# Kernel tuning notes

Hardware: AMD Instinct MI355X
Metric: run time of the kernel (lower is better)

The kernel has to match this reference:

```python
import jax, jax.numpy as jnp
import numpy as np

NUM_HEADS = 16
HEAD_DIM = 128  # 2048 / 16


def setup_inputs() -> dict:
    key = jax.random.key(0)
    ks = jax.random.split(key, 5)
    B, S, D = 2, 2048, 2048
    scale = 1.0 / np.sqrt(D)
    return {
        "x": jax.random.normal(ks[0], (B, S, D), dtype=jnp.float32),
        "Wq": jax.random.normal(ks[1], (D, D), dtype=jnp.float32) * scale,
        "Wk": jax.random.normal(ks[2], (D, D), dtype=jnp.float32) * scale,
        "Wv": jax.random.normal(ks[3], (D, D), dtype=jnp.float32) * scale,
        "Wo": jax.random.normal(ks[4], (D, D), dtype=jnp.float32) * scale,
    }


def reference(x, Wq, Wk, Wv, Wo):
    B, S, D = x.shape
    H, Hd = NUM_HEADS, HEAD_DIM
    # nn.Linear(bias=False): y = x @ W.T
    q = (x @ Wq.T).reshape(B, S, H, Hd).transpose(0, 2, 1, 3)  # [B,H,S,Hd]
    k = (x @ Wk.T).reshape(B, S, H, Hd).transpose(0, 2, 1, 3)
    v = (x @ Wv.T).reshape(B, S, H, Hd).transpose(0, 2, 1, 3)
    scores = jnp.einsum("bhqd,bhkd->bhqk", q, k) / jnp.sqrt(jnp.float32(Hd))
    attn = jax.nn.softmax(scores, axis=-1)  # dropout p=0 (eval) -> identity
    out = jnp.einsum("bhqk,bhkd->bhqd", attn, v)  # [B,H,S,Hd]
    out = out.transpose(0, 2, 1, 3).reshape(B, S, D)
    out = out @ Wo.T
    return out
```

## Files before the change

### kernel.cpp

```cpp
#include <hip/hip_runtime.h>
#include <math.h>
#include <stdint.h>


#define DDIM 2048
#define SEQ  2048
#define NH   16
#define HD   128

typedef __attribute__((ext_vector_type(4))) float f32x4;
typedef __attribute__((ext_vector_type(16))) float f32x16;
typedef __attribute__((ext_vector_type(8))) __bf16 bf16x8;
typedef __attribute__((ext_vector_type(4))) unsigned int u32x4;
typedef __attribute__((ext_vector_type(2))) unsigned int u32x2;

#define MFMA_B16(a, b, c) __builtin_amdgcn_mfma_f32_16x16x32_bf16((a), (b), (c), 0, 0, 0)
#define MFMA32(a, b, c) __builtin_amdgcn_mfma_f32_32x32x16_bf16((a), (b), (c), 0, 0, 0)

__device__ __forceinline__ void async16(const void* g, void* l) {
  __builtin_amdgcn_global_load_lds(
      (const __attribute__((address_space(1))) unsigned int*)g,
      (__attribute__((address_space(3))) unsigned int*)l, 16, 0, 0);
}

__device__ __forceinline__ unsigned short f2bf(float f) {
  unsigned u = __builtin_bit_cast(unsigned, f);
  u += 0x7fffu + ((u >> 16) & 1u);
  return (unsigned short)(u >> 16);
}

__device__ __forceinline__ bf16x8 ldfrag(const unsigned short* p) {
  return __builtin_bit_cast(bf16x8, *(const u32x4*)p);
}

__device__ __forceinline__ void cvt_body(const float* __restrict__ s,
                                         unsigned short* __restrict__ d, int i) {
  const f32x4* sp = (const f32x4*)s;
  f32x4 a = sp[2 * i], b = sp[2 * i + 1];
  u32x4 o;
  o.x = ((unsigned)f2bf(a.y) << 16) | f2bf(a.x);
  o.y = ((unsigned)f2bf(a.w) << 16) | f2bf(a.z);
  o.z = ((unsigned)f2bf(b.y) << 16) | f2bf(b.x);
  o.w = ((unsigned)f2bf(b.w) << 16) | f2bf(b.z);
  ((u32x4*)d)[i] = o;
}

__global__ __launch_bounds__(256) void cvt_bf16_kernel(const float* __restrict__ s,
                                                       unsigned short* __restrict__ d) {
  cvt_body(s, d, blockIdx.x * 256 + threadIdx.x);
}

__global__ __launch_bounds__(256) void cvt_all_kernel(const float* __restrict__ x,
                                                      const float* __restrict__ wq,
                                                      const float* __restrict__ wk,
                                                      const float* __restrict__ wv,
                                                      const float* __restrict__ wo,
                                                      unsigned short* __restrict__ xb,
                                                      unsigned short* __restrict__ wqkv,
                                                      unsigned short* __restrict__ wob) {
  const int b = blockIdx.x;
  if (b < 4096) {
    cvt_body(x, xb, b * 256 + threadIdx.x);
  } else if (b < 10240) {
    const int wi = (b - 4096) >> 11, lb = (b - 4096) & 2047;
    const float* s = (wi == 0) ? wq : (wi == 1) ? wk : wv;
    cvt_body(s, wqkv + (size_t)wi * 4194304u, lb * 256 + threadIdx.x);
  } else {
    cvt_body(wo, wob, (b - 10240) * 256 + threadIdx.x);
  }
}

__global__ __launch_bounds__(256) void gemm_qkv(const unsigned short* __restrict__ A,
                                                const unsigned short* __restrict__ B,
                                                unsigned short* __restrict__ Oqk,
                                                unsigned short* __restrict__ Ovt,
                                                float alpha_q) {
  __shared__ unsigned short As[128 * 64];
  __shared__ unsigned short Bs[128 * 64];
  const int tid = threadIdx.x;
  const int lane = tid & 63, w = tid >> 6;
  const int l32 = lane & 31, half = lane >> 5;
  const int wm = (w >> 1) * 64, wn = (w & 1) * 64;
  const int bm = blockIdx.y * 128, bn = blockIdx.x * 128;

  f32x16 acc[2][2];
#pragma unroll
  for (int i = 0; i < 2; ++i)
#pragma unroll
    for (int j = 0; j < 2; ++j)
#pragma unroll
      for (int e = 0; e < 16; ++e) acc[i][j][e] = 0.f;

  const unsigned short* pa[4];
  const unsigned short* pbb[4];
  {
#pragma unroll
    for (int j = 0; j < 4; ++j) {
      const int row = j * 32 + (tid >> 3);
      const int cg = (tid & 7) ^ (row & 7) ^ ((row >> 3) & 7);
      pa[j] = A + (size_t)(bm + row) * DDIM + cg * 8;
      pbb[j] = B + (size_t)(bn + row) * DDIM + cg * 8;
    }
  }

  const int fr = (l32 & 7) ^ (l32 >> 3);

  for (int kt = 0; kt < 32; ++kt) {
    __syncthreads();
#pragma unroll
    for (int j = 0; j < 4; ++j) {
      async16(pa[j], &As[(j * 256 + tid) * 8]);
      pa[j] += 64;
      async16(pbb[j], &Bs[(j * 256 + tid) * 8]);
      pbb[j] += 64;
    }
    __syncthreads();
#pragma unroll
    for (int ks = 0; ks < 4; ++ks) {
      const int ph = ks * 2 + half;
      const int sl0 = (ph ^ fr) * 8;
      const int sl1 = (ph ^ fr ^ 4) * 8;
      bf16x8 af0 = ldfrag(&As[(wm + l32) * 64 + sl0]);
      bf16x8 af1 = ldfrag(&As[(wm + 32 + l32) * 64 + sl1]);
      bf16x8 bf0 = ldfrag(&Bs[(wn + l32) * 64 + sl0]);
      bf16x8 bf1 = ldfrag(&Bs[(wn + 32 + l32) * 64 + sl1]);
      acc[0][0] = MFMA32(af0, bf0, acc[0][0]);
      acc[0][1] = MFMA32(af0, bf1, acc[0][1]);
      acc[1][0] = MFMA32(af1, bf0, acc[1][0]);
      acc[1][1] = MFMA32(af1, bf1, acc[1][1]);
    }
  }

  const int seg = bn >> 11;
  const int bnl = bn & 2047;
  const float alpha = (seg == 0) ? alpha_q : 1.0f;
#pragma unroll
  for (int i = 0; i < 2; ++i) {
#pragma unroll
    for (int j = 0; j < 2; ++j) {
#pragma unroll
      for (int rg = 0; rg < 4; ++rg) {
        const int m0 = bm + wm + i * 32 + rg * 8 + half * 4;
        const float v0 = acc[i][j][rg * 4 + 0] * alpha;
        const float v1 = acc[i][j][rg * 4 + 1] * alpha;
        const float v2 = acc[i][j][rg * 4 + 2] * alpha;
        const float v3 = acc[i][j][rg * 4 + 3] * alpha;
        const int n = bnl + wn + j * 32 + l32;
        if (seg < 2) {
          unsigned short* O = Oqk + (size_t)seg * (4096u * 2048u);
          O[(size_t)(m0 + 0) * DDIM + n] = f2bf(v0);
          O[(size_t)(m0 + 1) * DDIM + n] = f2bf(v1);
          O[(size_t)(m0 + 2) * DDIM + n] = f2bf(v2);
          O[(size_t)(m0 + 3) * DDIM + n] = f2bf(v3);
        } else {
          const int bb = m0 >> 11, s0 = m0 & 2047;
          const int hh = n >> 7, dd = n & 127;
          u32x2 st;
          st.x = ((unsigned)f2bf(v1) << 16) | f2bf(v0);
          st.y = ((unsigned)f2bf(v3) << 16) | f2bf(v2);
          *(u32x2*)&Ovt[((size_t)((bb * NH + hh) * HD + dd)) * SEQ + s0] = st;
        }
      }
    }
  }
}

__global__ __launch_bounds__(256) void gemm_o64(const unsigned short* __restrict__ A,
                                                const unsigned short* __restrict__ B,
                                                float* __restrict__ Cf) {
  __shared__ unsigned short As[128 * 64];
  __shared__ unsigned short Bs[64 * 64];
  const int tid = threadIdx.x;
  const int lane = tid & 63, w = tid >> 6;
  const int l32 = lane & 31, half = lane >> 5;
  const int wm = (w >> 1) * 64, wn = (w & 1) * 32;
  const int bm = blockIdx.y * 128, bn = blockIdx.x * 64;

  f32x16 acc[2];
#pragma unroll
  for (int i = 0; i < 2; ++i)
#pragma unroll
    for (int e = 0; e < 16; ++e) acc[i][e] = 0.f;

  const unsigned short* pa[4];
  const unsigned short* pbb[2];
  {
#pragma unroll
    for (int j = 0; j < 4; ++j) {
      const int row = j * 32 + (tid >> 3);
      const int cg = (tid & 7) ^ (row & 7) ^ ((row >> 3) & 7);
      pa[j] = A + (size_t)(bm + row) * DDIM + cg * 8;
      if (j < 2) pbb[j] = B + (size_t)(bn + row) * DDIM + cg * 8;
    }
  }

  const int fr = (l32 & 7) ^ (l32 >> 3);
  const int fb = fr ^ ((wn >> 3) & 4);

  for (int kt = 0; kt < 32; ++kt) {
    __syncthreads();
#pragma unroll
    for (int j = 0; j < 4; ++j) {
      async16(pa[j], &As[(j * 256 + tid) * 8]);
      pa[j] += 64;
      if (j < 2) {
        async16(pbb[j], &Bs[(j * 256 + tid) * 8]);
        pbb[j] += 64;
      }
    }
    __syncthreads();
#pragma unroll
    for (int ks = 0; ks < 4; ++ks) {
      const int ph = ks * 2 + half;
      bf16x8 af0 = ldfrag(&As[(wm + l32) * 64 + (ph ^ fr) * 8]);
      bf16x8 af1 = ldfrag(&As[(wm + 32 + l32) * 64 + (ph ^ fr ^ 4) * 8]);
      bf16x8 bf0 = ldfrag(&Bs[(wn + l32) * 64 + (ph ^ fb) * 8]);
      acc[0] = MFMA32(af0, bf0, acc[0]);
      acc[1] = MFMA32(af1, bf0, acc[1]);
    }
  }

#pragma unroll
  for (int i = 0; i < 2; ++i) {
#pragma unroll
    for (int rg = 0; rg < 4; ++rg) {
      const int m0 = bm + wm + i * 32 + rg * 8 + half * 4;
      const int n = bn + wn + l32;
      Cf[(size_t)(m0 + 0) * DDIM + n] = acc[i][rg * 4 + 0];
      Cf[(size_t)(m0 + 1) * DDIM + n] = acc[i][rg * 4 + 1];
      Cf[(size_t)(m0 + 2) * DDIM + n] = acc[i][rg * 4 + 2];
      Cf[(size_t)(m0 + 3) * DDIM + n] = acc[i][rg * 4 + 3];
    }
  }
}

__global__ __launch_bounds__(512) void attn_kernel(const unsigned short* __restrict__ qb,
                                                   const unsigned short* __restrict__ kb,
                                                   const unsigned short* __restrict__ vtb,
                                                   unsigned short* __restrict__ ab) {
  __shared__ unsigned short Ks[64 * 128];
  __shared__ unsigned short Vts[128 * 64];
  __shared__ unsigned short Pw[8 * 16 * 40];
  const int tid = threadIdx.x;
  const int w = tid >> 6, lane = tid & 63;
  const int quad = lane >> 4, l16 = lane & 15;
  const int qt = blockIdx.x, bh = blockIdx.y;
  const int b = bh >> 4, h = bh & 15;
  const int qrow = qt * 128 + w * 16 + l16;

  const unsigned short* qp = qb + ((size_t)(b * SEQ + qrow)) * DDIM + h * HD;
  bf16x8 qf[4];
#pragma unroll
  for (int ks = 0; ks < 4; ++ks) qf[ks] = ldfrag(qp + ks * 32 + quad * 8);

  f32x4 ot[8];
#pragma unroll
  for (int i = 0; i < 8; i++) ot[i] = f32x4{0.f, 0.f, 0.f, 0.f};
  float sumacc = 0.f;

  const unsigned short* kp[2];
  const unsigned short* vp[2];
  {
    const size_t kbase = ((size_t)(b * SEQ)) * DDIM + h * HD;
    const size_t vbase = ((size_t)((b * NH + h) * HD)) * SEQ;
#pragma unroll
    for (int j = 0; j < 2; ++j) {
      const int key = j * 32 + (tid >> 4), cgk = (tid & 15) ^ (key & 15);
      kp[j] = kb + kbase + (size_t)key * DDIM + cgk * 8;
      const int dd = j * 64 + (tid >> 3), cgv = (tid & 7) ^ (dd & 7);
      vp[j] = vtb + vbase + (size_t)dd * SEQ + cgv * 8;
    }
  }
  unsigned short* pw = &Pw[w * 640];

  for (int kt = 0; kt < SEQ / 64; ++kt) {
    __syncthreads();
#pragma unroll
    for (int j = 0; j < 2; ++j) {
      async16(kp[j], &Ks[(j * 512 + tid) * 8]);
      kp[j] += (size_t)64 * DDIM;
      async16(vp[j], &Vts[(j * 512 + tid) * 8]);
      vp[j] += 64;
    }
    __syncthreads();
    f32x4 s[4];
#pragma unroll
    for (int t = 0; t < 4; ++t) s[t] = f32x4{0.f, 0.f, 0.f, 0.f};
#pragma unroll
    for (int ks = 0; ks < 4; ++ks) {
      const int sl = ((ks * 4 + quad) ^ l16) * 8;
#pragma unroll
      for (int t = 0; t < 4; ++t) {
        bf16x8 a = ldfrag(&Ks[(t * 16 + l16) * 128 + sl]);
        s[t] = MFMA_B16(a, qf[ks], s[t]);
      }
    }
    f32x4 p[4];
#pragma unroll
    for (int t = 0; t < 4; ++t) {
      p[t].x = __builtin_amdgcn_exp2f(s[t].x);
      p[t].y = __builtin_amdgcn_exp2f(s[t].y);
      p[t].z = __builtin_amdgcn_exp2f(s[t].z);
      p[t].w = __builtin_amdgcn_exp2f(s[t].w);
      sumacc += (p[t].x + p[t].y) + (p[t].z + p[t].w);
    }
    bf16x8 pb0, pb1;
    {
      u32x2 w0, w1;
      w0.x = ((unsigned)f2bf(p[0].y) << 16) | f2bf(p[0].x);
      w0.y = ((unsigned)f2bf(p[0].w) << 16) | f2bf(p[0].z);
      w1.x = ((unsigned)f2bf(p[1].y) << 16) | f2bf(p[1].x);
      w1.y = ((unsigned)f2bf(p[1].w) << 16) | f2bf(p[1].z);
      *(u32x2*)&pw[l16 * 40 + quad * 4] = w0;
      *(u32x2*)&pw[l16 * 40 + 16 + quad * 4] = w1;
      asm volatile("s_waitcnt lgkmcnt(0)" ::: "memory");
      pb0 = ldfrag(&pw[l16 * 40 + quad * 8]);
      w0.x = ((unsigned)f2bf(p[2].y) << 16) | f2bf(p[2].x);
      w0.y = ((unsigned)f2bf(p[2].w) << 16) | f2bf(p[2].z);
      w1.x = ((unsigned)f2bf(p[3].y) << 16) | f2bf(p[3].x);
      w1.y = ((unsigned)f2bf(p[3].w) << 16) | f2bf(p[3].z);
      *(u32x2*)&pw[l16 * 40 + quad * 4] = w0;
      *(u32x2*)&pw[l16 * 40 + 16 + quad * 4] = w1;
      asm volatile("s_waitcnt lgkmcnt(0)" ::: "memory");
      pb1 = ldfrag(&pw[l16 * 40 + quad * 8]);
    }
#pragma unroll
    for (int mt = 0; mt < 8; ++mt) {
      bf16x8 vf0 = ldfrag(&Vts[(mt * 16 + l16) * 64 + (quad ^ (l16 & 7)) * 8]);
      ot[mt] = MFMA_B16(vf0, pb0, ot[mt]);
      bf16x8 vf1 = ldfrag(&Vts[(mt * 16 + l16) * 64 + ((4 + quad) ^ (l16 & 7)) * 8]);
      ot[mt] = MFMA_B16(vf1, pb1, ot[mt]);
    }
  }
  float total = sumacc;
  total += __shfl_xor(total, 16);
  total += __shfl_xor(total, 32);
  const float inv = 1.0f / total;
  unsigned short* op = ab + ((size_t)(b * SEQ + qrow)) * DDIM + h * HD;
#pragma unroll
  for (int mt = 0; mt < 8; ++mt) {
    f32x4 v = ot[mt] * inv;
    u32x2 st;
    st.x = ((unsigned)f2bf(v.y) << 16) | f2bf(v.x);
    st.y = ((unsigned)f2bf(v.w) << 16) | f2bf(v.z);
    *(u32x2*)&op[mt * 16 + quad * 4] = st;
  }
}

extern "C" void kernel_launch(void* const* d_in, const int* in_sizes, int n_in,
                              void* d_out, int out_size, void* d_ws, size_t ws_size,
                              hipStream_t stream) {
  (void)in_sizes; (void)n_in; (void)out_size;
  const float* x = (const float*)d_in[0];
  const float* Wq = (const float*)d_in[1];
  const float* Wk = (const float*)d_in[2];
  const float* Wv = (const float*)d_in[3];
  const float* Wo = (const float*)d_in[4];

  char* ws = (char*)d_ws;
  unsigned short* xb = (unsigned short*)(ws);
  unsigned short* wqkv = (unsigned short*)(ws + 16777216);
  unsigned short* qb = (unsigned short*)(ws + 41943040);
  unsigned short* kb = (unsigned short*)(ws + 58720256);
  unsigned short* vtb = (unsigned short*)(ws + 75497472);
  const bool big = ws_size >= 100663296ull;
  unsigned short* wob = big ? (unsigned short*)(ws + 92274688) : wqkv;

  const float alpha_q = 1.44269504088896341f / sqrtf(128.0f);

  if (big) {
    cvt_all_kernel<<<dim3(12288), 256, 0, stream>>>(x, Wq, Wk, Wv, Wo, xb, wqkv, wob);
    gemm_qkv<<<dim3(48, 32), 256, 0, stream>>>(xb, wqkv, qb, vtb, alpha_q);
  } else {
    cvt_all_kernel<<<dim3(10240), 256, 0, stream>>>(x, Wq, Wk, Wv, Wo, xb, wqkv, wob);
    gemm_qkv<<<dim3(48, 32), 256, 0, stream>>>(xb, wqkv, qb, vtb, alpha_q);
    cvt_bf16_kernel<<<dim3(2048), 256, 0, stream>>>(Wo, wob);
  }

  attn_kernel<<<dim3(16, 32), 512, 0, stream>>>(qb, kb, vtb, xb);

  gemm_o64<<<dim3(32, 32), 256, 0, stream>>>(xb, wob, (float*)d_out);
}
```

Baseline: 366.8 us.

## Rewrite QKV GEMM as 256x256 8-wave kernel with ping-pong LDS pipelining

```diff
diff --git a/kernel.cpp b/kernel.cpp
--- a/kernel.cpp
+++ b/kernel.cpp
@@ -70,82 +70,130 @@
   }
 }
 
-__global__ __launch_bounds__(256) void gemm_qkv(const unsigned short* __restrict__ A,
-                                                const unsigned short* __restrict__ B,
-                                                unsigned short* __restrict__ Oqk,
-                                                unsigned short* __restrict__ Ovt,
-                                                float alpha_q) {
-  __shared__ unsigned short As[128 * 64];
-  __shared__ unsigned short Bs[128 * 64];
+#define STGA(BUF, KH, COL)                            \
+  {                                                   \
+    const int c_ = (COL) & 2047;                      \
+    async16(pA[0] + c_, &As[BUF][KH][tid * 8]);       \
+    async16(pA[1] + c_, &As[BUF][KH][4096 + tid * 8]);\
+  }
+#define STGB(BUF, KH, COL)                            \
+  {                                                   \
+    const int c_ = (COL) & 2047;                      \
+    async16(pB[0] + c_, &Bs[BUF][KH][tid * 8]);       \
+    async16(pB[1] + c_, &Bs[BUF][KH][4096 + tid * 8]);\
+  }
+#define VM8 asm volatile("s_waitcnt vmcnt(8)" ::: "memory")
+#define VMNONE (void)0
+
+#define PHASE(BUF, KH, NH, STAGE_STMT, WAIT_STMT)                 \
+  {                                                               \
+    if ((NH) == 0) {                                              \
+      const unsigned short* pl = &As[BUF][KH][0];                 \
+      _Pragma("unroll") for (int mf = 0; mf < 4; ++mf) {          \
+        const int r = awbase + mf * 32;                           \
+        af[mf][0] = ldfrag(pl + r * 32 + c0);                     \
+        af[mf][1] = ldfrag(pl + r * 32 + c1);                     \
+      }                                                           \
+    }                                                             \
+    {                                                             \
+      const unsigned short* pl = &Bs[BUF][KH][0];                 \
+      const int r = bwbase + (NH) * 32;                           \
+      bf0 = ldfrag(pl + r * 32 + c0);                             \
+      bf1 = ldfrag(pl + r * 32 + c1);                             \
+    }                                                             \
+    STAGE_STMT;                                                   \
+    __builtin_amdgcn_s_barrier();                                 \
+    asm volatile("s_waitcnt lgkmcnt(0)" ::: "memory");            \
+    __builtin_amdgcn_sched_barrier(0);                            \
+    __builtin_amdgcn_s_setprio(1);                                \
+    _Pragma("unroll") for (int mf = 0; mf < 4; ++mf) {            \
+      acc[mf][NH] = MFMA32(af[mf][0], bf0, acc[mf][NH]);          \
+      acc[mf][NH] = MFMA32(af[mf][1], bf1, acc[mf][NH]);          \
+    }                                                             \
+    __builtin_amdgcn_s_setprio(0);                                \
+    WAIT_STMT;                                                    \
+    __builtin_amdgcn_s_barrier();                                 \
+  }
+
+__global__ __launch_bounds__(512) void gemm_qkv8(const unsigned short* __restrict__ A,
+                                                 const unsigned short* __restrict__ B,
+                                                 unsigned short* __restrict__ Oqk,
+                                                 unsigned short* __restrict__ Ovt,
+                                                 float alpha_q) {
+  __shared__ unsigned short As[2][2][256 * 32];
+  __shared__ unsigned short Bs[2][2][256 * 32];
   const int tid = threadIdx.x;
   const int lane = tid & 63, w = tid >> 6;
   const int l32 = lane & 31, half = lane >> 5;
-  const int wm = (w >> 1) * 64, wn = (w & 1) * 64;
-  const int bm = blockIdx.y * 128, bn = blockIdx.x * 128;
-
-  f32x16 acc[2][2];
-#pragma unroll
-  for (int i = 0; i < 2; ++i)
-#pragma unroll
-    for (int j = 0; j < 2; ++j)
-#pragma unroll
-      for (int e = 0; e < 16; ++e) acc[i][j][e] = 0.f;
-
-  const unsigned short* pa[4];
-  const unsigned short* pbb[4];
-  {
-#pragma unroll
-    for (int j = 0; j < 4; ++j) {
-      const int row = j * 32 + (tid >> 3);
-      const int cg = (tid & 7) ^ (row & 7) ^ ((row >> 3) & 7);
-      pa[j] = A + (size_t)(bm + row) * DDIM + cg * 8;
-      pbb[j] = B + (size_t)(bn + row) * DDIM + cg * 8;
-    }
-  }
-
-  const int fr = (l32 & 7) ^ (l32 >> 3);
-
-  for (int kt = 0; kt < 32; ++kt) {
-    __syncthreads();
-#pragma unroll
-    for (int j = 0; j < 4; ++j) {
-      async16(pa[j], &As[(j * 256 + tid) * 8]);
-      pa[j] += 64;
-      async16(pbb[j], &Bs[(j * 256 + tid) * 8]);
-      pbb[j] += 64;
-    }
-    __syncthreads();
-#pragma unroll
-    for (int ks = 0; ks < 4; ++ks) {
-      const int ph = ks * 2 + half;
-      const int sl0 = (ph ^ fr) * 8;
-      const int sl1 = (ph ^ fr ^ 4) * 8;
-      bf16x8 af0 = ldfrag(&As[(wm + l32) * 64 + sl0]);
-      bf16x8 af1 = ldfrag(&As[(wm + 32 + l32) * 64 + sl1]);
-      bf16x8 bf0 = ldfrag(&Bs[(wn + l32) * 64 + sl0]);
-      bf16x8 bf1 = ldfrag(&Bs[(wn + 32 + l32) * 64 + sl1]);
-      acc[0][0] = MFMA32(af0, bf0, acc[0][0]);
-      acc[0][1] = MFMA32(af0, bf1, acc[0][1]);
-      acc[1][0] = MFMA32(af1, bf0, acc[1][0]);
-      acc[1][1] = MFMA32(af1, bf1, acc[1][1]);
-    }
-  }
+  const int wr = w >> 2, wc = w & 3;
+  const int bm = blockIdx.y * 256, bn = blockIdx.x * 256;
+
+  const int f2 = (l32 >> 1) & 3;
+  const int c0 = (half ^ f2) * 8;
+  const int c1 = ((2 + half) ^ f2) * 8;
+  const int awbase = wr * 128 + l32;
+  const int bwbase = wc * 64 + l32;
+
+  f32x16 acc[4][2];
+#pragma unroll
+  for (int mf = 0; mf < 4; ++mf)
+#pragma unroll
+    for (int nf = 0; nf < 2; ++nf)
+#pragma unroll
+      for (int e = 0; e < 16; ++e) acc[mf][nf][e] = 0.f;
+
+  bf16x8 af[4][2];
+  bf16x8 bf0, bf1;
+
+  const unsigned short* pA[2];
+  const unsigned short* pB[2];
+#pragma unroll
+  for (int j = 0; j < 2; ++j) {
+    const int slot = j * 512 + tid;
+    const int row = slot >> 2, cs = slot & 3;
+    const int g = cs ^ ((row >> 1) & 3);
+    pA[j] = A + (size_t)(bm + row) * DDIM + g * 8;
+    pB[j] = B + (size_t)(bn + row) * DDIM + g * 8;
+  }
+
+  STGA(0, 0, 0);
+  STGB(0, 0, 0);
+  STGA(0, 1, 32);
+  STGB(0, 1, 32);
+  STGA(1, 0, 64);
+  STGB(1, 0, 64);
+  asm volatile("s_waitcnt vmcnt(8)" ::: "memory");
+  __builtin_amdgcn_s_barrier();
+
+#pragma unroll 1
+  for (int j = 0; j < 16; ++j) {
+    const int cb = j * 128;
+    PHASE(0, 0, 0, STGA(1, 1, cb + 96), VMNONE);
+    PHASE(0, 0, 1, STGB(1, 1, cb + 96), VM8);
+    PHASE(0, 1, 0, STGA(0, 0, cb + 128), VMNONE);
+    PHASE(0, 1, 1, STGB(0, 0, cb + 128), VM8);
+    PHASE(1, 0, 0, STGA(0, 1, cb + 160), VMNONE);
+    PHASE(1, 0, 1, STGB(0, 1, cb + 160), VM8);
+    PHASE(1, 1, 0, STGA(1, 0, cb + 192), VMNONE);
+    PHASE(1, 1, 1, STGB(1, 0, cb + 192), VM8);
+  }
+  asm volatile("s_waitcnt vmcnt(0)" ::: "memory");
 
   const int seg = bn >> 11;
   const int bnl = bn & 2047;
   const float alpha = (seg == 0) ? alpha_q : 1.0f;
 #pragma unroll
-  for (int i = 0; i < 2; ++i) {
-#pragma unroll
-    for (int j = 0; j < 2; ++j) {
+  for (int mf = 0; mf < 4; ++mf) {
+#pragma unroll
+    for (int nf = 0; nf < 2; ++nf) {
 #pragma unroll
       for (int rg = 0; rg < 4; ++rg) {
-        const int m0 = bm + wm + i * 32 + rg * 8 + half * 4;
-        const float v0 = acc[i][j][rg * 4 + 0] * alpha;
-        const float v1 = acc[i][j][rg * 4 + 1] * alpha;
-        const float v2 = acc[i][j][rg * 4 + 2] * alpha;
-        const float v3 = acc[i][j][rg * 4 + 3] * alpha;
-        const int n = bnl + wn + j * 32 + l32;
+        const int m0 = bm + wr * 128 + mf * 32 + rg * 8 + half * 4;
+        const float v0 = acc[mf][nf][rg * 4 + 0] * alpha;
+        const float v1 = acc[mf][nf][rg * 4 + 1] * alpha;
+        const float v2 = acc[mf][nf][rg * 4 + 2] * alpha;
+        const float v3 = acc[mf][nf][rg * 4 + 3] * alpha;
+        const int n = bnl + wc * 64 + nf * 32 + l32;
         if (seg < 2) {
           unsigned short* O = Oqk + (size_t)seg * (4096u * 2048u);
           O[(size_t)(m0 + 0) * DDIM + n] = f2bf(v0);
@@ -370,10 +418,10 @@
 
   if (big) {
     cvt_all_kernel<<<dim3(12288), 256, 0, stream>>>(x, Wq, Wk, Wv, Wo, xb, wqkv, wob);
-    gemm_qkv<<<dim3(48, 32), 256, 0, stream>>>(xb, wqkv, qb, vtb, alpha_q);
+    gemm_qkv8<<<dim3(24, 16), 512, 0, stream>>>(xb, wqkv, qb, vtb, alpha_q);
   } else {
     cvt_all_kernel<<<dim3(10240), 256, 0, stream>>>(x, Wq, Wk, Wv, Wo, xb, wqkv, wob);
-    gemm_qkv<<<dim3(48, 32), 256, 0, stream>>>(xb, wqkv, qb, vtb, alpha_q);
+    gemm_qkv8<<<dim3(24, 16), 512, 0, stream>>>(xb, wqkv, qb, vtb, alpha_q);
     cvt_bf16_kernel<<<dim3(2048), 256, 0, stream>>>(Wo, wob);
   }
 
```

Result: slower. 411.4 us (+12.2%).
